# Kernel tuning notes

Measured on AMD Instinct MI355X. Metric: run time of the kernel, lower is better.

The kernel has to match this reference:

```python
import jax, jax.numpy as jnp
import numpy as np

N = 100000      # nodes
E = 6400000     # edges (avg degree 64)
S = 8           # FSM states
X = 2 ** S      # neighborhood 'characters' (256)
ITERS = 20      # NeuralFSM.iterations


def setup_inputs() -> dict:
    key = jax.random.key(0)
    k1, k2, k3 = jax.random.split(key, 3)
    # one-hot initial node states [N, S]
    state_idx = jax.random.randint(k1, (N,), 0, S)
    s0 = jax.nn.one_hot(state_idx, S, dtype=jnp.float32)
    # edge list [2, E]
    edge_index = jax.random.randint(k2, (2, E), 0, N, dtype=jnp.int32)
    # FSM transition tensor T[char, state, :] is one-hot over next state -> [X, S, S]
    next_state = jax.random.randint(k3, (X, S), 0, S)
    T = jax.nn.one_hot(next_state, S, dtype=jnp.float32)
    return {"s0": s0, "edge_index": edge_index, "T": T}


def reference(s0, edge_index, T):
    n_nodes, n_states = s0.shape
    src, dst = edge_index[0], edge_index[1]
    powers = (2 ** jnp.arange(n_states)).astype(jnp.int32)  # base-2 encoding of thresholded aggr

    def step(s, _):
        # message = x_j gathered from source nodes, scatter-added at destinations
        msg_sum = jax.ops.segment_sum(s[src], dst, num_segments=n_nodes)  # [N, S]
        # threshold (> 0.5) then clamp to {0,1}
        aggr = (msg_sum > 0.5).astype(jnp.int32)                          # [N, S]
        # multiple-hot -> index into 2^S characters (one-hot folded into a gather)
        idx = aggr @ powers                                               # [N]
        # einsum('x,s,xst->t') with one-hot char == gather T[idx] then contract state
        new_s = jnp.einsum('ns,nst->nt', s, T[idx])                       # [N, S]
        return new_s, None

    s_final, _ = jax.lax.scan(step, s0, None, length=ITERS)
    return s_final
```

## Files before the change

kernel.cpp:

```cpp
#include <hip/hip_runtime.h>
#include <hip/hip_bf16.h>
#include <stdint.h>


#define NN 100000
#define EE 6400000
#define NCHARS 2048
#define ITERS 20

#define NBKT 250
#define NPB 400
#define WPS 12500
#define X4N 3125
#define CEDGE 12800
#define NCHUNK 500
#define CAPB 27648
#define HCAP 13824

#define MEG_TOP     2080
#define CUR_OFF     3328
#define BAR_WORDS   4096

typedef uint32_t u32x4 __attribute__((ext_vector_type(4)));

__device__ inline void mega_barrier(uint32_t* bar, int line, uint32_t epoch) {
    __syncthreads();
    if (threadIdx.x == 0) {
        uint32_t old = atomicAdd(&bar[1664 + line * 16], 1u);
        if (old + 1u == 10u * epoch) {
            uint32_t told = atomicAdd(&bar[MEG_TOP], 1u);
            if (told + 1u == 25u * epoch) {
                for (int r = 0; r < 25; ++r)
                    atomicExch(&bar[2112 + r * 16], epoch);
            }
        }
        while (__hip_atomic_load(&bar[2112 + line * 16], __ATOMIC_RELAXED,
                                 __HIP_MEMORY_SCOPE_AGENT) < epoch)
            __builtin_amdgcn_s_sleep(1);
    }
    __syncthreads();
}

__global__ void __launch_bounds__(512) build_kernel(const int* __restrict__ src,
                                                    const int* __restrict__ dst,
                                                    const float* __restrict__ s0,
                                                    const float* __restrict__ T,
                                                    uint32_t* __restrict__ gPk0,
                                                    uint8_t* __restrict__ nextT,
                                                    uint32_t* __restrict__ csr,
                                                    uint32_t* __restrict__ bar) {
    __shared__ uint32_t stage[CEDGE];
    __shared__ uint32_t cw[8][256];
    __shared__ uint32_t scanb[512];
    __shared__ uint32_t loc[NBKT + 1];
    __shared__ uint32_t segoff[NBKT];
    __shared__ uint8_t  lut[CEDGE];
    int t = threadIdx.x, w = t >> 6;
    int c = blockIdx.x;
    int e0 = c * CEDGE;
    const int4* ps4 = (const int4*)(src + e0);
    const int4* pd4 = (const int4*)(dst + e0);
    uint32_t* cursorG = bar + CUR_OFF;

    if (t < 25) loc[t] = 0;
    __syncthreads();
    if (t < 200) {
        const float* row = s0 + ((size_t)c * 200 + t) * 8;
        int s = 0;
        #pragma unroll
        for (int q = 1; q < 8; ++q) if (row[q] > 0.5f) s = q;
        atomicOr(&loc[t >> 3], (uint32_t)s << ((t & 7) << 2));
    }
    __syncthreads();
    if (t < 25) gPk0[c * 25 + t] = loc[t];
    if (c < 4) {
        const float* row = T + (c * 512 + t) * 8;
        int s = 0;
        #pragma unroll
        for (int q = 1; q < 8; ++q) if (row[q] > 0.5f) s = q;
        nextT[c * 512 + t] = (uint8_t)s;
    }
    __syncthreads();

    for (int i = t; i < 8 * 256; i += 512) ((uint32_t*)cw)[i] = 0;
    __syncthreads();
    for (int i = t; i < CEDGE / 4; i += 512) {
        int4 d = pd4[i];
        atomicAdd(&cw[w][d.x / NPB], 1u);
        atomicAdd(&cw[w][d.y / NPB], 1u);
        atomicAdd(&cw[w][d.z / NPB], 1u);
        atomicAdd(&cw[w][d.w / NPB], 1u);
    }
    __syncthreads();
    uint32_t tot = 0;
    if (t < NBKT) {
        #pragma unroll
        for (int w2 = 0; w2 < 8; ++w2) tot += cw[w2][t];
    }
    scanb[t] = tot;
    __syncthreads();
    for (int off = 1; off < 512; off <<= 1) {
        uint32_t x = (t >= off) ? scanb[t - off] : 0u;
        __syncthreads();
        scanb[t] += x;
        __syncthreads();
    }
    if (t < NBKT) {
        uint32_t excl = scanb[t] - tot;
        loc[t] = excl;
        uint32_t myStart = atomicAdd(&cursorG[t], tot);
        segoff[t] = (uint32_t)t * CAPB + myStart - excl;
        uint32_t acc = excl;
        #pragma unroll
        for (int w2 = 0; w2 < 8; ++w2) {
            uint32_t cv = cw[w2][t];
            cw[w2][t] = acc;
            acc += cv;
        }
    }
    if (t == 0) loc[NBKT] = CEDGE;
    __syncthreads();
    for (int b = t; b < NBKT; b += 512) {
        uint32_t lo = loc[b], hi = loc[b + 1];
        for (uint32_t i = lo; i < hi; ++i) lut[i] = (uint8_t)b;
    }
    for (int i = t; i < CEDGE / 4; i += 512) {
        int4 d = pd4[i];
        int4 s = ps4[i];
        int bb; uint32_t dl, pos;
        bb = d.x / NPB; dl = (uint32_t)(d.x - bb * NPB);
        pos = atomicAdd(&cw[w][bb], 1u);
        stage[pos] = ((uint32_t)(s.x >> 3) << 18) | ((uint32_t)(s.x & 7) << 13) | (dl << 2);
        bb = d.y / NPB; dl = (uint32_t)(d.y - bb * NPB);
        pos = atomicAdd(&cw[w][bb], 1u);
        stage[pos] = ((uint32_t)(s.y >> 3) << 18) | ((uint32_t)(s.y & 7) << 13) | (dl << 2);
        bb = d.z / NPB; dl = (uint32_t)(d.z - bb * NPB);
        pos = atomicAdd(&cw[w][bb], 1u);
        stage[pos] = ((uint32_t)(s.z >> 3) << 18) | ((uint32_t)(s.z & 7) << 13) | (dl << 2);
        bb = d.w / NPB; dl = (uint32_t)(d.w - bb * NPB);
        pos = atomicAdd(&cw[w][bb], 1u);
        stage[pos] = ((uint32_t)(s.w >> 3) << 18) | ((uint32_t)(s.w & 7) << 13) | (dl << 2);
    }
    __syncthreads();
    for (int i = t; i < CEDGE; i += 512) {
        csr[segoff[lut[i]] + (uint32_t)i] = stage[i];
    }
}

__global__ void __launch_bounds__(512) p4_sortsrc(uint32_t* __restrict__ csr,
                                                  const uint32_t* __restrict__ cntG) {
    __shared__ uint32_t ob[HCAP];
    __shared__ uint32_t binh[512];
    int t = threadIdx.x;
    int j = blockIdx.x;
    int b = j >> 1, h = j & 1;
    uint32_t n  = cntG[b];
    uint32_t n1 = (((n + 1) >> 1) + 255u) & ~255u;
    if (n1 > n) n1 = n;
    uint32_t r0 = (uint32_t)b * CAPB + (h ? n1 : 0);
    uint32_t cnt = h ? n - n1 : n1;
    if (cnt == 0 || cnt > HCAP) return;
    binh[t] = 0;
    __syncthreads();
    for (uint32_t i = t; i < cnt; i += 512) atomicAdd(&binh[csr[r0 + i] >> 23], 1u);
    __syncthreads();
    uint32_t v = binh[t];
    __syncthreads();
    for (int off = 1; off < 512; off <<= 1) {
        uint32_t x = (t >= off) ? binh[t - off] : 0u;
        __syncthreads();
        binh[t] += x;
        __syncthreads();
    }
    uint32_t excl = binh[t] - v;
    __syncthreads();
    binh[t] = excl;
    __syncthreads();
    for (uint32_t i = t; i < cnt; i += 512) {
        uint32_t w = csr[r0 + i];
        uint32_t pos = atomicAdd(&binh[w >> 23], 1u);
        ob[pos] = w;
    }
    __syncthreads();
    for (uint32_t i = t; i < cnt; i += 512) {
        uint32_t s = ((i | 255u) < cnt)
                   ? ((i & ~255u) | ((i & 3u) << 6) | ((i & 255u) >> 2))
                   : i;
        csr[r0 + i] = ob[s];
    }
}

__global__ void __launch_bounds__(1024) mega_kernel(const uint32_t* __restrict__ csr,
                                                    uint32_t* __restrict__ gPkA,
                                                    uint32_t* __restrict__ gPkB,
                                                    const uint8_t* __restrict__ nextT,
                                                    float* __restrict__ out,
                                                    uint32_t* __restrict__ bar) {
    __shared__ uint32_t sPk[WPS];
    __shared__ uint32_t mask[NPB];
    __shared__ uint32_t packOwn[NPB / 8];
    __shared__ uint8_t  nT[NCHARS];
    __shared__ uint8_t  sown[NPB];
    int t = threadIdx.x;
    int b = blockIdx.x;
    uint32_t base = (uint32_t)b * CAPB;
    uint32_t end  = base + bar[CUR_OFF + b];

    if (t < 512) ((uint32_t*)nT)[t] = ((const uint32_t*)nextT)[t];
    const int line = b % 25;

    for (int p = 0; p < ITERS; ++p) {
        const uint32_t* curG = (p & 1) ? gPkB : gPkA;
        uint32_t*       nxtG = (p & 1) ? gPkA : gPkB;
        {
            const u32x4* g4 = (const u32x4*)curG;
            int i0 = t, i1 = t + 1024, i2 = t + 2048;
            int i3 = t + 3072; if (i3 > X4N - 1) i3 = X4N - 1;
            const u32x4 *p0 = g4 + i0, *p1 = g4 + i1, *p2 = g4 + i2, *p3 = g4 + i3;
            u32x4 a0, a1, a2, a3;
            asm volatile(
                "global_load_dwordx4 %0, %4, off sc1\n\t"
                "global_load_dwordx4 %1, %5, off sc1\n\t"
                "global_load_dwordx4 %2, %6, off sc1\n\t"
                "global_load_dwordx4 %3, %7, off sc1\n\t"
                "s_waitcnt vmcnt(0)"
                : "=&v"(a0), "=&v"(a1), "=&v"(a2), "=&v"(a3)
                : "v"(p0), "v"(p1), "v"(p2), "v"(p3)
                : "memory");
            u32x4* s4 = (u32x4*)sPk;
            s4[i0] = a0; s4[i1] = a1; s4[i2] = a2; s4[i3] = a3;
        }
        if (t < NPB) mask[t] = 0;
        if (t < NPB / 8) packOwn[t] = 0;
        __syncthreads();

        auto edge1 = [&](uint32_t wv) {
            uint32_t val = *(const uint32_t*)((const char*)sPk + (wv >> 16));
            uint32_t nb  = (val >> ((wv >> 11) & 31u)) & 7u;
            atomicOr((uint32_t*)((char*)mask + (wv & 0x7FCu)), 1u << nb);
        };
        uint32_t e = base + ((uint32_t)t << 2);
        for (; e + 4099 < end; e += 8192) {
            u32x4 wa = *(const u32x4*)(csr + e);
            u32x4 wb = *(const u32x4*)(csr + e + 4096);
            edge1(wa.x); edge1(wa.y); edge1(wa.z); edge1(wa.w);
            edge1(wb.x); edge1(wb.y); edge1(wb.z); edge1(wb.w);
        }
        for (; e + 3 < end; e += 4096) {
            u32x4 wa = *(const u32x4*)(csr + e);
            edge1(wa.x); edge1(wa.y); edge1(wa.z); edge1(wa.w);
        }
        for (; e < end; ++e) {
            edge1(csr[e]);
        }
        __syncthreads();

        if (t < NPB) {
            int node = b * NPB + t;
            uint32_t sOwn = (sPk[node >> 3] >> ((node & 7) << 2)) & 7u;
            uint8_t ns = nT[(mask[t] << 3) + sOwn];
            sown[t] = ns;
            atomicOr(&packOwn[t >> 3], (uint32_t)ns << ((t & 7) << 2));
        }
        __syncthreads();
        if (p < ITERS - 1) {
            if (t < NPB / 8)
                __hip_atomic_store(&nxtG[(NPB / 8) * b + t], packOwn[t],
                                   __ATOMIC_RELAXED, __HIP_MEMORY_SCOPE_AGENT);
            mega_barrier(bar, line, (uint32_t)(p + 1));
        }
    }
    __syncthreads();
    for (int f = t; f < NPB * 8; f += 1024) {
        int node = f >> 3;
        out[(size_t)b * (NPB * 8) + f] = ((f & 7) == (int)sown[node]) ? 1.f : 0.f;
    }
}

__global__ void fb_decode(const float* __restrict__ s0, const float* __restrict__ T,
                          uint8_t* __restrict__ state, uint8_t* __restrict__ nextT,
                          uint32_t* __restrict__ mask) {
    int i = blockIdx.x * blockDim.x + threadIdx.x;
    if (i < NCHARS) {
        const float* row = T + i * 8;
        int t = 0;
        #pragma unroll
        for (int k = 1; k < 8; ++k) if (row[k] > 0.5f) t = k;
        nextT[i] = (uint8_t)t;
    }
    if (i < NN) {
        const float* row = s0 + i * 8;
        int s = 0;
        #pragma unroll
        for (int k = 1; k < 8; ++k) if (row[k] > 0.5f) s = k;
        state[i] = (uint8_t)s;
        mask[i] = 0u;
    }
}
__global__ void fb_edge(const int* __restrict__ src, const int* __restrict__ dst,
                        const uint8_t* __restrict__ state, uint32_t* __restrict__ mask) {
    int i = blockIdx.x * blockDim.x + threadIdx.x;
    int stride = gridDim.x * blockDim.x;
    for (int e = i; e < EE; e += stride) atomicOr(&mask[dst[e]], 1u << state[src[e]]);
}
__global__ void fb_update(uint8_t* __restrict__ state, uint32_t* __restrict__ mask,
                          const uint8_t* __restrict__ nextT) {
    int i = blockIdx.x * blockDim.x + threadIdx.x;
    if (i < NN) {
        uint32_t m = mask[i];
        state[i] = nextT[(m << 3) + state[i]];
        mask[i] = 0u;
    }
}
__global__ void fb_output(const uint8_t* __restrict__ state, float* __restrict__ out) {
    int i = blockIdx.x * blockDim.x + threadIdx.x;
    if (i < NN) {
        int s = state[i];
        float4 lo = make_float4(s == 0 ? 1.f : 0.f, s == 1 ? 1.f : 0.f,
                                s == 2 ? 1.f : 0.f, s == 3 ? 1.f : 0.f);
        float4 hi = make_float4(s == 4 ? 1.f : 0.f, s == 5 ? 1.f : 0.f,
                                s == 6 ? 1.f : 0.f, s == 7 ? 1.f : 0.f);
        float4* o = (float4*)(out + (size_t)i * 8);
        o[0] = lo;
        o[1] = hi;
    }
}

extern "C" void kernel_launch(void* const* d_in, const int* in_sizes, int n_in,
                              void* d_out, int out_size, void* d_ws, size_t ws_size,
                              hipStream_t stream) {
    const float* s0  = (const float*)d_in[0];
    const int*   ei  = (const int*)d_in[1];
    const float* T   = (const float*)d_in[2];
    float*       out = (float*)d_out;
    const int* src = ei;
    const int* dst = ei + EE;

    uint8_t* basep = (uint8_t*)d_ws;
    size_t off = 0;
    auto alloc = [&](size_t sz) -> void* {
        void* p = basep + off;
        off += (sz + 255) & ~(size_t)255;
        return p;
    };
    uint32_t* csr   = (uint32_t*)alloc(sizeof(uint32_t) * (size_t)NBKT * CAPB);
    uint8_t*  nextT = (uint8_t*)alloc(NCHARS);
    uint32_t* gPkA  = (uint32_t*)alloc(sizeof(uint32_t) * WPS);
    uint32_t* gPkB  = (uint32_t*)alloc(sizeof(uint32_t) * WPS);
    uint32_t* bar   = (uint32_t*)alloc(sizeof(uint32_t) * BAR_WORDS);
    bool have_ws = (off <= ws_size);

    if (have_ws) {
        hipMemsetAsync(bar, 0, sizeof(uint32_t) * BAR_WORDS, stream);
        build_kernel<<<NCHUNK, 512, 0, stream>>>(src, dst, s0, T, gPkA, nextT, csr, bar);
        p4_sortsrc<<<NBKT * 2, 512, 0, stream>>>(csr, bar + CUR_OFF);
        mega_kernel<<<NBKT, 1024, 0, stream>>>(csr, gPkA, gPkB, nextT, out, bar);
    } else {
        uint32_t* mask = (uint32_t*)d_ws;
        uint8_t*  nT   = (uint8_t*)d_ws + 400128;
        uint8_t*  st   = (uint8_t*)d_ws + 402432;
        fb_decode<<<391, 256, 0, stream>>>(s0, T, st, nT, mask);
        for (int it = 0; it < ITERS; ++it) {
            fb_edge<<<2048, 256, 0, stream>>>(src, dst, st, mask);
            fb_update<<<391, 256, 0, stream>>>(st, mask, nT);
        }
        fb_output<<<391, 256, 0, stream>>>(st, out);
    }
}
```

Before: 247.2 us.

## Split each destination bucket across two 512-thread persistent blocks by destination half

The sort pass now processes a whole bucket per block, keying edges by destination half (local node index below or above 200) plus source, and records the split point for later use. The persistent mega kernel launches 500 blocks of 512 threads instead of 250 of 1024, with each block owning half a bucket's nodes and edges and writing its own slice of packed state and output. The grid barrier counts are updated to match. This spreads the per-iteration edge work over more, smaller blocks that may co-reside per CU. In exchange each block must reload the full packed state every iteration, doubling that traffic, and the barrier has more participants.

```diff
diff --git a/kernel.cpp b/kernel.cpp
--- a/kernel.cpp
+++ b/kernel.cpp
@@ -9,16 +9,18 @@
 #define ITERS 20
 
 #define NBKT 250
+#define MBLK 500
 #define NPB 400
+#define NPH 200
 #define WPS 12500
 #define X4N 3125
 #define CEDGE 12800
 #define NCHUNK 500
 #define CAPB 27648
-#define HCAP 13824
 
 #define MEG_TOP     2080
 #define CUR_OFF     3328
+#define HCNT_OFF    3584
 #define BAR_WORDS   4096
 
 typedef uint32_t u32x4 __attribute__((ext_vector_type(4)));
@@ -27,7 +29,7 @@
     __syncthreads();
     if (threadIdx.x == 0) {
         uint32_t old = atomicAdd(&bar[1664 + line * 16], 1u);
-        if (old + 1u == 10u * epoch) {
+        if (old + 1u == 20u * epoch) {
             uint32_t told = atomicAdd(&bar[MEG_TOP], 1u);
             if (told + 1u == 25u * epoch) {
                 for (int r = 0; r < 25; ++r)
@@ -148,115 +150,137 @@
 }
 
 __global__ void __launch_bounds__(512) p4_sortsrc(uint32_t* __restrict__ csr,
-                                                  const uint32_t* __restrict__ cntG) {
-    __shared__ uint32_t ob[HCAP];
+                                                  uint32_t* __restrict__ bar) {
+    __shared__ uint32_t ob[CAPB];
     __shared__ uint32_t binh[512];
+    __shared__ uint32_t Hs;
+    int t = threadIdx.x;
+    int b = blockIdx.x;
+    uint32_t n  = bar[CUR_OFF + b];
+    if (n > CAPB) n = CAPB;
+    uint32_t r0 = (uint32_t)b * CAPB;
+    auto key = [](uint32_t w) {
+        return (((w & 0x7FCu) >= 0x320u) ? 256u : 0u) | (w >> 24);
+    };
+    binh[t] = 0;
+    __syncthreads();
+    for (uint32_t i = t; i < n; i += 512) atomicAdd(&binh[key(csr[r0 + i])], 1u);
+    __syncthreads();
+    uint32_t v = binh[t];
+    __syncthreads();
+    for (int off = 1; off < 512; off <<= 1) {
+        uint32_t x = (t >= off) ? binh[t - off] : 0u;
+        __syncthreads();
+        binh[t] += x;
+        __syncthreads();
+    }
+    uint32_t excl = binh[t] - v;
+    if (t == 255) {
+        Hs = binh[t];
+        bar[HCNT_OFF + b] = binh[t];
+    }
+    __syncthreads();
+    binh[t] = excl;
+    __syncthreads();
+    for (uint32_t i = t; i < n; i += 512) {
+        uint32_t w = csr[r0 + i];
+        uint32_t pos = atomicAdd(&binh[key(w)], 1u);
+        ob[pos] = w;
+    }
+    __syncthreads();
+    uint32_t H = Hs;
+    for (uint32_t i = t; i < n; i += 512) {
+        uint32_t bf = i & ~255u, bl = i | 255u;
+        bool full = (bl < n);
+        bool straddle = (bf < H) && (bl >= H);
+        uint32_t s = (full && !straddle)
+                   ? (bf | ((i & 3u) << 6) | ((i & 255u) >> 2))
+                   : i;
+        csr[r0 + i] = ob[s];
+    }
+}
+
+__global__ void __launch_bounds__(512, 4) mega_kernel(const uint32_t* __restrict__ csr,
+                                                      uint32_t* __restrict__ gPkA,
+                                                      uint32_t* __restrict__ gPkB,
+                                                      const uint8_t* __restrict__ nextT,
+                                                      float* __restrict__ out,
+                                                      uint32_t* __restrict__ bar) {
+    __shared__ uint32_t sPk[WPS];
+    __shared__ uint32_t mask[NPH];
+    __shared__ uint32_t packOwn[NPH / 8];
+    __shared__ uint8_t  nT[NCHARS];
+    __shared__ uint8_t  sown[NPH];
     int t = threadIdx.x;
     int j = blockIdx.x;
     int b = j >> 1, h = j & 1;
-    uint32_t n  = cntG[b];
-    uint32_t n1 = (((n + 1) >> 1) + 255u) & ~255u;
-    if (n1 > n) n1 = n;
-    uint32_t r0 = (uint32_t)b * CAPB + (h ? n1 : 0);
-    uint32_t cnt = h ? n - n1 : n1;
-    if (cnt == 0 || cnt > HCAP) return;
-    binh[t] = 0;
-    __syncthreads();
-    for (uint32_t i = t; i < cnt; i += 512) atomicAdd(&binh[csr[r0 + i] >> 23], 1u);
-    __syncthreads();
-    uint32_t v = binh[t];
-    __syncthreads();
-    for (int off = 1; off < 512; off <<= 1) {
-        uint32_t x = (t >= off) ? binh[t - off] : 0u;
-        __syncthreads();
-        binh[t] += x;
-        __syncthreads();
-    }
-    uint32_t excl = binh[t] - v;
-    __syncthreads();
-    binh[t] = excl;
-    __syncthreads();
-    for (uint32_t i = t; i < cnt; i += 512) {
-        uint32_t w = csr[r0 + i];
-        uint32_t pos = atomicAdd(&binh[w >> 23], 1u);
-        ob[pos] = w;
-    }
-    __syncthreads();
-    for (uint32_t i = t; i < cnt; i += 512) {
-        uint32_t s = ((i | 255u) < cnt)
-                   ? ((i & ~255u) | ((i & 3u) << 6) | ((i & 255u) >> 2))
-                   : i;
-        csr[r0 + i] = ob[s];
-    }
-}
-
-__global__ void __launch_bounds__(1024) mega_kernel(const uint32_t* __restrict__ csr,
-                                                    uint32_t* __restrict__ gPkA,
-                                                    uint32_t* __restrict__ gPkB,
-                                                    const uint8_t* __restrict__ nextT,
-                                                    float* __restrict__ out,
-                                                    uint32_t* __restrict__ bar) {
-    __shared__ uint32_t sPk[WPS];
-    __shared__ uint32_t mask[NPB];
-    __shared__ uint32_t packOwn[NPB / 8];
-    __shared__ uint8_t  nT[NCHARS];
-    __shared__ uint8_t  sown[NPB];
-    int t = threadIdx.x;
-    int b = blockIdx.x;
-    uint32_t base = (uint32_t)b * CAPB;
-    uint32_t end  = base + bar[CUR_OFF + b];
-
-    if (t < 512) ((uint32_t*)nT)[t] = ((const uint32_t*)nextT)[t];
-    const int line = b % 25;
+    uint32_t r0 = (uint32_t)b * CAPB;
+    uint32_t n  = bar[CUR_OFF + b];
+    uint32_t H  = bar[HCNT_OFF + b];
+    if (H > n) H = n;
+    uint32_t lo = r0 + (h ? H : 0);
+    uint32_t hi = r0 + (h ? n : H);
+    uint32_t A0 = (lo + 255u) & ~255u;
+    if (A0 > hi) A0 = hi;
+    uint32_t hoff = h ? 800u : 0u;
+    const int line = j % 25;
+
+    ((uint32_t*)nT)[t] = ((const uint32_t*)nextT)[t];
 
     for (int p = 0; p < ITERS; ++p) {
         const uint32_t* curG = (p & 1) ? gPkB : gPkA;
         uint32_t*       nxtG = (p & 1) ? gPkA : gPkB;
         {
             const u32x4* g4 = (const u32x4*)curG;
-            int i0 = t, i1 = t + 1024, i2 = t + 2048;
-            int i3 = t + 3072; if (i3 > X4N - 1) i3 = X4N - 1;
-            const u32x4 *p0 = g4 + i0, *p1 = g4 + i1, *p2 = g4 + i2, *p3 = g4 + i3;
-            u32x4 a0, a1, a2, a3;
+            int i0 = t, i1 = t + 512, i2 = t + 1024, i3 = t + 1536;
+            int i4 = t + 2048, i5 = t + 2560, i6 = t + 3072;
+            if (i6 > X4N - 1) i6 = X4N - 1;
+            const u32x4 *q0 = g4 + i0, *q1 = g4 + i1, *q2 = g4 + i2, *q3 = g4 + i3;
+            const u32x4 *q4 = g4 + i4, *q5 = g4 + i5, *q6 = g4 + i6;
+            u32x4 a0, a1, a2, a3, a4, a5, a6;
             asm volatile(
-                "global_load_dwordx4 %0, %4, off sc1\n\t"
-                "global_load_dwordx4 %1, %5, off sc1\n\t"
-                "global_load_dwordx4 %2, %6, off sc1\n\t"
-                "global_load_dwordx4 %3, %7, off sc1\n\t"
+                "global_load_dwordx4 %0, %7, off sc1\n\t"
+                "global_load_dwordx4 %1, %8, off sc1\n\t"
+                "global_load_dwordx4 %2, %9, off sc1\n\t"
+                "global_load_dwordx4 %3, %10, off sc1\n\t"
+                "global_load_dwordx4 %4, %11, off sc1\n\t"
+                "global_load_dwordx4 %5, %12, off sc1\n\t"
+                "global_load_dwordx4 %6, %13, off sc1\n\t"
                 "s_waitcnt vmcnt(0)"
-                : "=&v"(a0), "=&v"(a1), "=&v"(a2), "=&v"(a3)
-                : "v"(p0), "v"(p1), "v"(p2), "v"(p3)
+                : "=&v"(a0), "=&v"(a1), "=&v"(a2), "=&v"(a3),
+                  "=&v"(a4), "=&v"(a5), "=&v"(a6)
+                : "v"(q0), "v"(q1), "v"(q2), "v"(q3), "v"(q4), "v"(q5), "v"(q6)
                 : "memory");
             u32x4* s4 = (u32x4*)sPk;
             s4[i0] = a0; s4[i1] = a1; s4[i2] = a2; s4[i3] = a3;
-        }
-        if (t < NPB) mask[t] = 0;
-        if (t < NPB / 8) packOwn[t] = 0;
+            s4[i4] = a4; s4[i5] = a5; s4[i6] = a6;
+        }
+        if (t < NPH) mask[t] = 0;
+        if (t < NPH / 8) packOwn[t] = 0;
         __syncthreads();
 
         auto edge1 = [&](uint32_t wv) {
             uint32_t val = *(const uint32_t*)((const char*)sPk + (wv >> 16));
             uint32_t nb  = (val >> ((wv >> 11) & 31u)) & 7u;
-            atomicOr((uint32_t*)((char*)mask + (wv & 0x7FCu)), 1u << nb);
+            atomicOr((uint32_t*)((char*)mask + (wv & 0x7FCu) - hoff), 1u << nb);
         };
-        uint32_t e = base + ((uint32_t)t << 2);
-        for (; e + 4099 < end; e += 8192) {
+        for (uint32_t i = lo + (uint32_t)t; i < A0; i += 512) edge1(csr[i]);
+        uint32_t e = A0 + ((uint32_t)t << 2);
+        for (; e + 2051 < hi; e += 4096) {
             u32x4 wa = *(const u32x4*)(csr + e);
-            u32x4 wb = *(const u32x4*)(csr + e + 4096);
+            u32x4 wb = *(const u32x4*)(csr + e + 2048);
             edge1(wa.x); edge1(wa.y); edge1(wa.z); edge1(wa.w);
             edge1(wb.x); edge1(wb.y); edge1(wb.z); edge1(wb.w);
         }
-        for (; e + 3 < end; e += 4096) {
+        for (; e + 3 < hi; e += 2048) {
             u32x4 wa = *(const u32x4*)(csr + e);
             edge1(wa.x); edge1(wa.y); edge1(wa.z); edge1(wa.w);
         }
-        for (; e < end; ++e) {
-            edge1(csr[e]);
-        }
-        __syncthreads();
-
-        if (t < NPB) {
-            int node = b * NPB + t;
+        for (; e < hi; ++e) edge1(csr[e]);
+        __syncthreads();
+
+        if (t < NPH) {
+            int node = b * NPB + h * NPH + t;
             uint32_t sOwn = (sPk[node >> 3] >> ((node & 7) << 2)) & 7u;
             uint8_t ns = nT[(mask[t] << 3) + sOwn];
             sown[t] = ns;
@@ -264,16 +288,16 @@
         }
         __syncthreads();
         if (p < ITERS - 1) {
-            if (t < NPB / 8)
-                __hip_atomic_store(&nxtG[(NPB / 8) * b + t], packOwn[t],
+            if (t < NPH / 8)
+                __hip_atomic_store(&nxtG[50 * b + 25 * h + t], packOwn[t],
                                    __ATOMIC_RELAXED, __HIP_MEMORY_SCOPE_AGENT);
             mega_barrier(bar, line, (uint32_t)(p + 1));
         }
     }
     __syncthreads();
-    for (int f = t; f < NPB * 8; f += 1024) {
+    for (int f = t; f < NPH * 8; f += 512) {
         int node = f >> 3;
-        out[(size_t)b * (NPB * 8) + f] = ((f & 7) == (int)sown[node]) ? 1.f : 0.f;
+        out[(size_t)(b * NPB + h * NPH) * 8 + f] = ((f & 7) == (int)sown[node]) ? 1.f : 0.f;
     }
 }
 
@@ -353,8 +377,8 @@
     if (have_ws) {
         hipMemsetAsync(bar, 0, sizeof(uint32_t) * BAR_WORDS, stream);
         build_kernel<<<NCHUNK, 512, 0, stream>>>(src, dst, s0, T, gPkA, nextT, csr, bar);
-        p4_sortsrc<<<NBKT * 2, 512, 0, stream>>>(csr, bar + CUR_OFF);
-        mega_kernel<<<NBKT, 1024, 0, stream>>>(csr, gPkA, gPkB, nextT, out, bar);
+        p4_sortsrc<<<NBKT, 512, 0, stream>>>(csr, bar);
+        mega_kernel<<<MBLK, 512, 0, stream>>>(csr, gPkA, gPkB, nextT, out, bar);
     } else {
         uint32_t* mask = (uint32_t*)d_ws;
         uint8_t*  nT   = (uint8_t*)d_ws + 400128;
```

Result: slower. 279.3 us (+13.0%).
